# Performance work log

Hardware: AMD Instinct MI355X
Metric: run time of the kernel (lower is better)

The kernel has to match this reference:

```python
import jax, jax.numpy as jnp
import numpy as np

B, N, C_IN, C_OUT, M = 32, 4096, 128, 128, 256


def setup_inputs() -> dict:
    key = jax.random.key(0)
    k1, k2, k3, k4 = jax.random.split(key, 4)
    x = jax.random.normal(k1, (B, N, C_IN), dtype=jnp.float32)
    # Lowest-M eigenvectors of a graph Laplacian are orthonormal columns [N, M];
    # build an equivalent orthonormal basis via QR of a random matrix.
    U, _ = jnp.linalg.qr(jax.random.normal(k2, (N, M), dtype=jnp.float32))
    # complex spectral weights ~ 0.02 * randn (cfloat) split into real/imag parts
    W_real = jax.random.normal(k3, (C_IN, C_OUT, M), dtype=jnp.float32) * 0.02
    W_imag = jax.random.normal(k4, (C_IN, C_OUT, M), dtype=jnp.float32) * 0.02
    return {"x": x, "eigenvectors": U, "W_real": W_real, "W_imag": W_imag}


def reference(x, eigenvectors, W_real, W_imag):
    # Graph Fourier transform: project node features onto spectral modes.
    # x_spec[b, m, c] = sum_n U[n, m] * x[b, n, c]
    x_spec = jnp.einsum('nm,bnc->bmc', eigenvectors, x)  # [B, M, C_in], real
    # Per-mode complex channel mixing, fused into one batched einsum.
    # Original takes .real of (x_spec * W); since x_spec is real,
    # Re(x_spec @ W) = x_spec @ Re(W), so W_imag does not affect the output.
    out_spec_real = jnp.einsum('bmc,com->bmo', x_spec, W_real)  # [B, M, C_out]
    # Inverse graph Fourier transform back to node space.
    return jnp.einsum('nm,bmo->bno', eigenvectors, out_spec_real)  # [B, N, C_out]
```

## Files before the change

### kernel.cpp

```cpp
#include <hip/hip_runtime.h>
#include <hip/hip_bf16.h>

#define BB 32
#define NN 4096
#define CI 128
#define CO 128
#define MM 256
#define KS 8

typedef __hip_bfloat16 bf16;
typedef __attribute__((ext_vector_type(8))) short bf16x8;
typedef __attribute__((ext_vector_type(4))) float f32x4;

__device__ inline void gl_lds16(const void* g, void* l) {
    __builtin_amdgcn_global_load_lds(
        (const __attribute__((address_space(1))) void*)g,
        (__attribute__((address_space(3))) void*)l, 16, 0, 0);
}

__global__ __launch_bounds__(256) void k_cvtU(const float* __restrict__ U,
                                              bf16* __restrict__ Un,
                                              bf16* __restrict__ Ut) {
    const int n0 = blockIdx.x * 64;
    const int m0 = blockIdx.y * 64;
    __shared__ float tile[64][65];
    const int t = threadIdx.x;
    #pragma unroll
    for (int i = 0; i < 16; ++i) {
        int lin = t + i * 256;
        int r = lin >> 6, c = lin & 63;
        float v = U[(n0 + r) * MM + m0 + c];
        tile[r][c] = v;
        Un[(n0 + r) * MM + m0 + c] = __float2bfloat16(v);
    }
    __syncthreads();
    #pragma unroll
    for (int pass = 0; pass < 2; ++pass) {
        int no = t & 7;
        int m  = (t >> 3) + pass * 32;
        bf16 tmp[8];
        #pragma unroll
        for (int j = 0; j < 8; ++j) tmp[j] = __float2bfloat16(tile[no * 8 + j][m]);
        *(bf16x8*)&Ut[(long)(m0 + m) * NN + n0 + no * 8] = *(bf16x8*)tmp;
    }
}

__global__ __launch_bounds__(256) void k_trx(const float* __restrict__ x,
                                             bf16* __restrict__ xT) {
    const int c0 = blockIdx.x * 64;
    const int n0 = blockIdx.y * 64;
    const int b  = blockIdx.z;
    __shared__ float tile[64][65];
    const int t = threadIdx.x;
    #pragma unroll
    for (int pass = 0; pass < 4; ++pass) {
        int r  = (t >> 4) + pass * 16;
        int c4 = (t & 15) * 4;
        float4 v = *(const float4*)&x[((long)b * NN + n0 + r) * CI + c0 + c4];
        tile[r][c4 + 0] = v.x; tile[r][c4 + 1] = v.y;
        tile[r][c4 + 2] = v.z; tile[r][c4 + 3] = v.w;
    }
    __syncthreads();
    #pragma unroll
    for (int pass = 0; pass < 2; ++pass) {
        int no = t & 7;
        int c  = (t >> 3) + pass * 32;
        bf16 tmp[8];
        #pragma unroll
        for (int j = 0; j < 8; ++j) tmp[j] = __float2bfloat16(tile[no * 8 + j][c]);
        *(bf16x8*)&xT[((long)b * CI + c0 + c) * NN + n0 + no * 8] = *(bf16x8*)tmp;
    }
}

__global__ __launch_bounds__(256) void k_wt(const float* __restrict__ W,
                                            bf16* __restrict__ Wt) {
    const int m0 = blockIdx.x * 64;
    const int o0 = blockIdx.y * 64;
    const int c  = blockIdx.z;
    __shared__ float tile[64][65];
    const int t = threadIdx.x;
    #pragma unroll
    for (int pass = 0; pass < 4; ++pass) {
        int r  = (t >> 4) + pass * 16;
        int m4 = (t & 15) * 4;
        float4 v = *(const float4*)&W[((long)c * CO + o0 + r) * MM + m0 + m4];
        tile[r][m4 + 0] = v.x; tile[r][m4 + 1] = v.y;
        tile[r][m4 + 2] = v.z; tile[r][m4 + 3] = v.w;
    }
    __syncthreads();
    #pragma unroll
    for (int pass = 0; pass < 2; ++pass) {
        int oo = t & 7;
        int m  = (t >> 3) + pass * 32;
        bf16 tmp[8];
        #pragma unroll
        for (int j = 0; j < 8; ++j) tmp[j] = __float2bfloat16(tile[oo * 8 + j][m]);
        *(bf16x8*)&Wt[((long)(m0 + m) * CI + c) * CO + o0 + oo * 8] = *(bf16x8*)tmp;
    }
}

__global__ __launch_bounds__(256) void k_gemm1(const bf16* __restrict__ Ut,
                                               const bf16* __restrict__ xT,
                                               bf16* __restrict__ part) {
    const int ks = blockIdx.x;
    const int m0 = blockIdx.y * 128;
    const int b  = blockIdx.z;
    __shared__ __align__(16) bf16 As[128 * 32];
    __shared__ __align__(16) bf16 Bs[128 * 32];
    const int t    = threadIdx.x;
    const int lane = t & 63;
    const int wave = t >> 6;
    const int wm   = wave >> 1, wn = wave & 1;
    const int fr   = lane & 15;
    const int kg   = (lane >> 4) * 8;
    f32x4 acc[4][4] = {};
    const long xbase = (long)b * CI * NN;
    for (int kt = 0; kt < 512 / 32; ++kt) {
        const int k0 = ks * 512 + kt * 32;
        #pragma unroll
        for (int i = 0; i < 2; ++i) {
            int lin = t + i * 256;
            int r = lin >> 2, kk = (lin & 3) * 8;
            gl_lds16(&Ut[(long)(m0 + r) * NN + k0 + kk], &As[lin * 8]);
            gl_lds16(&xT[xbase + (long)r * NN + k0 + kk], &Bs[lin * 8]);
        }
        __syncthreads();
        bf16x8 a[4], bfr[4];
        #pragma unroll
        for (int i = 0; i < 4; ++i)
            a[i] = *(const bf16x8*)&As[(wm * 64 + i * 16 + fr) * 32 + kg];
        #pragma unroll
        for (int j = 0; j < 4; ++j)
            bfr[j] = *(const bf16x8*)&Bs[(wn * 64 + j * 16 + fr) * 32 + kg];
        #pragma unroll
        for (int i = 0; i < 4; ++i)
            #pragma unroll
            for (int j = 0; j < 4; ++j)
                acc[i][j] = __builtin_amdgcn_mfma_f32_16x16x32_bf16(a[i], bfr[j], acc[i][j], 0, 0, 0);
        __syncthreads();
    }
    const int quad = (lane >> 4) * 4;
    const long pbase = ((long)ks * BB + b) * MM * CI;
    #pragma unroll
    for (int i = 0; i < 4; ++i) {
        #pragma unroll
        for (int j = 0; j < 4; ++j) {
            int mg = m0 + wm * 64 + i * 16 + quad;
            int cg = wn * 64 + j * 16 + fr;
            #pragma unroll
            for (int r = 0; r < 4; ++r)
                part[pbase + (long)(mg + r) * CI + cg] = __float2bfloat16(acc[i][j][r]);
        }
    }
}

__global__ __launch_bounds__(256) void k_mix(const bf16* __restrict__ part,
                                             const bf16* __restrict__ Wt,
                                             bf16* __restrict__ osT) {
    const int blk = blockIdx.x;
    const int mi  = blk >> 1;
    const int m   = (mi & 7) * 32 + (mi >> 3);
    const int o0  = (blk & 1) * 64;
    __shared__ float Wl[CI][64];
    __shared__ float xl[CI][36];
    const int t = threadIdx.x;
    const long wb = (long)m * CI * CO;
    #pragma unroll
    for (int i = 0; i < 4; ++i) {
        int ch = t + i * 256;
        int c = ch >> 3, og = (ch & 7) * 8;
        bf16x8 v = *(const bf16x8*)&Wt[wb + (long)c * CO + o0 + og];
        #pragma unroll
        for (int j = 0; j < 8; ++j) Wl[c][og + j] = __bfloat162float(((const bf16*)&v)[j]);
    }
    #pragma unroll
    for (int i = 0; i < 2; ++i) {
        int ch = t + i * 256;
        int b = ch >> 4, c8 = (ch & 15) * 8;
        float s[8] = {};
        #pragma unroll
        for (int ks = 0; ks < KS; ++ks) {
            bf16x8 v = *(const bf16x8*)&part[(((long)ks * BB + b) * MM + m) * CI + c8];
            #pragma unroll
            for (int j = 0; j < 8; ++j) s[j] += __bfloat162float(((const bf16*)&v)[j]);
        }
        #pragma unroll
        for (int j = 0; j < 8; ++j) xl[c8 + j][b] = s[j];
    }
    __syncthreads();
    const int op = t & 63;
    const int bq = t >> 6;
    float acc[8] = {};
    for (int c = 0; c < CI; ++c) {
        float w = Wl[c][op];
        #pragma unroll
        for (int j = 0; j < 8; ++j)
            acc[j] += xl[c][bq * 8 + j] * w;
    }
    #pragma unroll
    for (int j = 0; j < 8; ++j)
        osT[((long)(bq * 8 + j) * CO + o0 + op) * MM + m] = __float2bfloat16(acc[j]);
}

__global__ __launch_bounds__(256) void k_gemm3(const bf16* __restrict__ Un,
                                               const bf16* __restrict__ osT,
                                               float* __restrict__ out) {
    const int n0 = blockIdx.x * 128;
    const int b  = blockIdx.y;
    __shared__ __align__(16) bf16 As[128 * 32];
    __shared__ __align__(16) bf16 Bs[128 * 32];
    const int t    = threadIdx.x;
    const int lane = t & 63;
    const int wave = t >> 6;
    const int wm   = wave >> 1, wn = wave & 1;
    const int fr   = lane & 15;
    const int kg   = (lane >> 4) * 8;
    f32x4 acc[4][4] = {};
    const long bbase = (long)b * CO * MM;
    for (int kt = 0; kt < MM / 32; ++kt) {
        const int k0 = kt * 32;
        #pragma unroll
        for (int i = 0; i < 2; ++i) {
            int lin = t + i * 256;
            int r = lin >> 2, kk = (lin & 3) * 8;
            gl_lds16(&Un[(long)(n0 + r) * MM + k0 + kk], &As[lin * 8]);
            gl_lds16(&osT[bbase + (long)r * MM + k0 + kk], &Bs[lin * 8]);
        }
        __syncthreads();
        bf16x8 a[4], bfr[4];
        #pragma unroll
        for (int i = 0; i < 4; ++i)
            a[i] = *(const bf16x8*)&As[(wm * 64 + i * 16 + fr) * 32 + kg];
        #pragma unroll
        for (int j = 0; j < 4; ++j)
            bfr[j] = *(const bf16x8*)&Bs[(wn * 64 + j * 16 + fr) * 32 + kg];
        #pragma unroll
        for (int i = 0; i < 4; ++i)
            #pragma unroll
            for (int j = 0; j < 4; ++j)
                acc[i][j] = __builtin_amdgcn_mfma_f32_16x16x32_bf16(a[i], bfr[j], acc[i][j], 0, 0, 0);
        __syncthreads();
    }
    const int quad = (lane >> 4) * 4;
    #pragma unroll
    for (int i = 0; i < 4; ++i) {
        #pragma unroll
        for (int j = 0; j < 4; ++j) {
            int ng = n0 + wm * 64 + i * 16 + quad;
            int og = wn * 64 + j * 16 + fr;
            #pragma unroll
            for (int r = 0; r < 4; ++r)
                out[((long)b * NN + ng + r) * CO + og] = acc[i][j][r];
        }
    }
}

extern "C" void kernel_launch(void* const* d_in, const int* in_sizes, int n_in,
                              void* d_out, int out_size, void* d_ws, size_t ws_size,
                              hipStream_t stream) {
    const float* x  = (const float*)d_in[0];
    const float* U  = (const float*)d_in[1];
    const float* Wr = (const float*)d_in[2];
    float* out = (float*)d_out;

    char* p = (char*)d_ws;
    bf16* xT   = (bf16*)p;  p += (size_t)BB * CI * NN * 2;
    bf16* part = (bf16*)p;  p += (size_t)KS * BB * MM * CI * 2;
    bf16* Ut   = (bf16*)p;  p += (size_t)MM * NN * 2;
    bf16* Un   = (bf16*)p;  p += (size_t)NN * MM * 2;
    bf16* osT  = (bf16*)p;  p += (size_t)BB * CO * MM * 2;
    bf16* Wt   = (bf16*)p;  p += (size_t)MM * CI * CO * 2;

    k_cvtU <<<dim3(NN / 64, MM / 64), 256, 0, stream>>>(U, Un, Ut);
    k_trx  <<<dim3(CI / 64, NN / 64, BB), 256, 0, stream>>>(x, xT);
    k_wt   <<<dim3(MM / 64, CO / 64, CI), 256, 0, stream>>>(Wr, Wt);
    k_gemm1<<<dim3(KS, MM / 128, BB), 256, 0, stream>>>(Ut, xT, part);
    k_mix  <<<dim3(512), 256, 0, stream>>>(part, Wt, osT);
    k_gemm3<<<dim3(NN / 128, BB), 256, 0, stream>>>(Un, osT, out);
}
```

Measured before the change: 201.0 us.

## Fuse x transpose-convert into double-buffered GEMM1 and widen mix blocks

Removes the separate transpose/convert kernel for x. GEMM1 now loads fp32 x tiles straight into LDS and converts and transposes them to bf16 in-kernel. Each 512-thread GEMM1 block covers all 256 modes with double-buffered LDS staging, so the grid shrinks to 256 blocks. The mix kernel handles all 128 output channels per block with bf16 weights in LDS and 16 accumulators per thread. This cuts a full round trip of x through HBM and one launch, at the cost of fewer blocks in GEMM1, heavier LDS use and more register pressure.

New measurement: 187.7 us. 6.6% less time.

```diff
diff --git a/kernel.cpp b/kernel.cpp
--- a/kernel.cpp
+++ b/kernel.cpp
@@ -45,33 +45,6 @@
     }
 }
 
-__global__ __launch_bounds__(256) void k_trx(const float* __restrict__ x,
-                                             bf16* __restrict__ xT) {
-    const int c0 = blockIdx.x * 64;
-    const int n0 = blockIdx.y * 64;
-    const int b  = blockIdx.z;
-    __shared__ float tile[64][65];
-    const int t = threadIdx.x;
-    #pragma unroll
-    for (int pass = 0; pass < 4; ++pass) {
-        int r  = (t >> 4) + pass * 16;
-        int c4 = (t & 15) * 4;
-        float4 v = *(const float4*)&x[((long)b * NN + n0 + r) * CI + c0 + c4];
-        tile[r][c4 + 0] = v.x; tile[r][c4 + 1] = v.y;
-        tile[r][c4 + 2] = v.z; tile[r][c4 + 3] = v.w;
-    }
-    __syncthreads();
-    #pragma unroll
-    for (int pass = 0; pass < 2; ++pass) {
-        int no = t & 7;
-        int c  = (t >> 3) + pass * 32;
-        bf16 tmp[8];
-        #pragma unroll
-        for (int j = 0; j < 8; ++j) tmp[j] = __float2bfloat16(tile[no * 8 + j][c]);
-        *(bf16x8*)&xT[((long)b * CI + c0 + c) * NN + n0 + no * 8] = *(bf16x8*)tmp;
-    }
-}
-
 __global__ __launch_bounds__(256) void k_wt(const float* __restrict__ W,
                                             bf16* __restrict__ Wt) {
     const int m0 = blockIdx.x * 64;
@@ -99,14 +72,14 @@
     }
 }
 
-__global__ __launch_bounds__(256) void k_gemm1(const bf16* __restrict__ Ut,
-                                               const bf16* __restrict__ xT,
-                                               bf16* __restrict__ part) {
+__global__ __launch_bounds__(512) void k_gemm1f(const bf16* __restrict__ Ut,
+                                                const float* __restrict__ x,
+                                                bf16* __restrict__ part) {
     const int ks = blockIdx.x;
-    const int m0 = blockIdx.y * 128;
-    const int b  = blockIdx.z;
-    __shared__ __align__(16) bf16 As[128 * 32];
-    __shared__ __align__(16) bf16 Bs[128 * 32];
+    const int b  = blockIdx.y;
+    __shared__ __align__(16) bf16  As[2][MM * 32];
+    __shared__ __align__(16) bf16  Bs[2][CI * 32];
+    __shared__ __align__(16) float Xf[2][32 * CI];
     const int t    = threadIdx.x;
     const int lane = t & 63;
     const int wave = t >> 6;
@@ -114,24 +87,49 @@
     const int fr   = lane & 15;
     const int kg   = (lane >> 4) * 8;
     f32x4 acc[4][4] = {};
-    const long xbase = (long)b * CI * NN;
-    for (int kt = 0; kt < 512 / 32; ++kt) {
-        const int k0 = ks * 512 + kt * 32;
+    const long xrow  = (long)b * NN;
+    const int  kbase = ks * 512;
+
+    auto STAGE = [&](int buf, int kt) {
+        const int k0 = kbase + kt * 32;
         #pragma unroll
         for (int i = 0; i < 2; ++i) {
-            int lin = t + i * 256;
-            int r = lin >> 2, kk = (lin & 3) * 8;
-            gl_lds16(&Ut[(long)(m0 + r) * NN + k0 + kk], &As[lin * 8]);
-            gl_lds16(&xT[xbase + (long)r * NN + k0 + kk], &Bs[lin * 8]);
+            int lin = t + i * 512;
+            {
+                int r = lin >> 2, kk = (lin & 3) * 8;
+                gl_lds16(&Ut[(long)r * NN + k0 + kk], &As[buf][lin * 8]);
+            }
+            {
+                int r = lin >> 5, c4 = (lin & 31) * 4;
+                gl_lds16(&x[(xrow + k0 + r) * CI + c4], &Xf[buf][lin * 4]);
+            }
+        }
+    };
+
+    const int NT = 512 / 32;
+    STAGE(0, 0);
+    __syncthreads();
+    #pragma unroll
+    for (int kt = 0; kt < NT; ++kt) {
+        const int cur = kt & 1;
+        if (kt + 1 < NT) STAGE(cur ^ 1, kt + 1);
+        {
+            const int c  = t & 127;
+            const int nh = t >> 7;
+            bf16 tmp[8];
+            #pragma unroll
+            for (int j = 0; j < 8; ++j)
+                tmp[j] = __float2bfloat16(Xf[cur][(nh * 8 + j) * CI + c]);
+            *(bf16x8*)&Bs[cur][c * 32 + nh * 8] = *(bf16x8*)tmp;
         }
         __syncthreads();
         bf16x8 a[4], bfr[4];
         #pragma unroll
         for (int i = 0; i < 4; ++i)
-            a[i] = *(const bf16x8*)&As[(wm * 64 + i * 16 + fr) * 32 + kg];
+            a[i] = *(const bf16x8*)&As[cur][(wm * 64 + i * 16 + fr) * 32 + kg];
         #pragma unroll
         for (int j = 0; j < 4; ++j)
-            bfr[j] = *(const bf16x8*)&Bs[(wn * 64 + j * 16 + fr) * 32 + kg];
+            bfr[j] = *(const bf16x8*)&Bs[cur][(wn * 64 + j * 16 + fr) * 32 + kg];
         #pragma unroll
         for (int i = 0; i < 4; ++i)
             #pragma unroll
@@ -145,7 +143,7 @@
     for (int i = 0; i < 4; ++i) {
         #pragma unroll
         for (int j = 0; j < 4; ++j) {
-            int mg = m0 + wm * 64 + i * 16 + quad;
+            int mg = wm * 64 + i * 16 + quad;
             int cg = wn * 64 + j * 16 + fr;
             #pragma unroll
             for (int r = 0; r < 4; ++r)
@@ -158,20 +156,16 @@
                                              const bf16* __restrict__ Wt,
                                              bf16* __restrict__ osT) {
     const int blk = blockIdx.x;
-    const int mi  = blk >> 1;
-    const int m   = (mi & 7) * 32 + (mi >> 3);
-    const int o0  = (blk & 1) * 64;
-    __shared__ float Wl[CI][64];
+    const int m   = (blk & 7) * 32 + (blk >> 3);
+    __shared__ bf16  Wl[CI][CO];
     __shared__ float xl[CI][36];
     const int t = threadIdx.x;
     const long wb = (long)m * CI * CO;
     #pragma unroll
-    for (int i = 0; i < 4; ++i) {
+    for (int i = 0; i < 8; ++i) {
         int ch = t + i * 256;
-        int c = ch >> 3, og = (ch & 7) * 8;
-        bf16x8 v = *(const bf16x8*)&Wt[wb + (long)c * CO + o0 + og];
-        #pragma unroll
-        for (int j = 0; j < 8; ++j) Wl[c][og + j] = __bfloat162float(((const bf16*)&v)[j]);
+        int c = ch >> 4, og = (ch & 15) * 8;
+        *(bf16x8*)&Wl[c][og] = *(const bf16x8*)&Wt[wb + (long)c * CO + og];
     }
     #pragma unroll
     for (int i = 0; i < 2; ++i) {
@@ -188,18 +182,18 @@
         for (int j = 0; j < 8; ++j) xl[c8 + j][b] = s[j];
     }
     __syncthreads();
-    const int op = t & 63;
-    const int bq = t >> 6;
-    float acc[8] = {};
+    const int o  = t & 127;
+    const int bh = t >> 7;
+    float acc[16] = {};
     for (int c = 0; c < CI; ++c) {
-        float w = Wl[c][op];
-        #pragma unroll
-        for (int j = 0; j < 8; ++j)
-            acc[j] += xl[c][bq * 8 + j] * w;
-    }
-    #pragma unroll
-    for (int j = 0; j < 8; ++j)
-        osT[((long)(bq * 8 + j) * CO + o0 + op) * MM + m] = __float2bfloat16(acc[j]);
+        float w = __bfloat162float(Wl[c][o]);
+        #pragma unroll
+        for (int j = 0; j < 16; ++j)
+            acc[j] += xl[c][bh * 16 + j] * w;
+    }
+    #pragma unroll
+    for (int j = 0; j < 16; ++j)
+        osT[((long)(bh * 16 + j) * CO + o) * MM + m] = __float2bfloat16(acc[j]);
 }
 
 __global__ __launch_bounds__(256) void k_gemm3(const bf16* __restrict__ Un,
@@ -264,17 +258,15 @@
     float* out = (float*)d_out;
 
     char* p = (char*)d_ws;
-    bf16* xT   = (bf16*)p;  p += (size_t)BB * CI * NN * 2;
     bf16* part = (bf16*)p;  p += (size_t)KS * BB * MM * CI * 2;
     bf16* Ut   = (bf16*)p;  p += (size_t)MM * NN * 2;
     bf16* Un   = (bf16*)p;  p += (size_t)NN * MM * 2;
     bf16* osT  = (bf16*)p;  p += (size_t)BB * CO * MM * 2;
     bf16* Wt   = (bf16*)p;  p += (size_t)MM * CI * CO * 2;
 
-    k_cvtU <<<dim3(NN / 64, MM / 64), 256, 0, stream>>>(U, Un, Ut);
-    k_trx  <<<dim3(CI / 64, NN / 64, BB), 256, 0, stream>>>(x, xT);
-    k_wt   <<<dim3(MM / 64, CO / 64, CI), 256, 0, stream>>>(Wr, Wt);
-    k_gemm1<<<dim3(KS, MM / 128, BB), 256, 0, stream>>>(Ut, xT, part);
-    k_mix  <<<dim3(512), 256, 0, stream>>>(part, Wt, osT);
-    k_gemm3<<<dim3(NN / 128, BB), 256, 0, stream>>>(Un, osT, out);
-}
+    k_cvtU  <<<dim3(NN / 64, MM / 64), 256, 0, stream>>>(U, Un, Ut);
+    k_wt    <<<dim3(MM / 64, CO / 64, CI), 256, 0, stream>>>(Wr, Wt);
+    k_gemm1f<<<dim3(KS, BB), 512, 0, stream>>>(Ut, x, part);
+    k_mix   <<<dim3(256), 256, 0, stream>>>(part, Wt, osT);
+    k_gemm3 <<<dim3(NN / 128, BB), 256, 0, stream>>>(Un, osT, out);
+}
```
